# Kernel tuning notes

Measured on AMD Instinct MI355X. Metric: run time of the kernel, lower is better.

## Reference

```python
import jax, jax.numpy as jnp
import numpy as np

QMIN_A, QMAX_A = -128, 127  # int8 activation range
GROUPSIZE = 32


def per_token_quant_dequant(x):
    """Dynamic per-token asymmetric int8 fake-quant (torchao per_token_dynamic_quant)."""
    min_val = jnp.minimum(jnp.min(x, axis=-1, keepdims=True), 0.0)
    max_val = jnp.maximum(jnp.max(x, axis=-1, keepdims=True), 0.0)
    scale = (max_val - min_val) / float(QMAX_A - QMIN_A)
    scale = jnp.maximum(scale, jnp.finfo(x.dtype).eps)
    zp = jnp.clip(QMIN_A - jnp.round(min_val / scale), QMIN_A, QMAX_A)
    q = jnp.clip(jnp.round(x / scale) + zp, QMIN_A, QMAX_A)
    return (q - zp) * scale


def dequant_int4_grouped(w_int, w_scales, w_zeros):
    """w_int: [O, I] int4 values in [-8, 7]; scales/zeros: [O, I//GROUPSIZE]."""
    O, I = w_int.shape
    G = I // GROUPSIZE
    wg = w_int.reshape(O, G, GROUPSIZE).astype(w_scales.dtype)
    w_dq = (wg - w_zeros[:, :, None]) * w_scales[:, :, None]
    return w_dq.reshape(O, I)


def setup_inputs() -> dict:
    key = jax.random.key(0)
    k1, k2, k3 = jax.random.split(key, 3)
    B, S, D_IN, D_OUT = 4, 2048, 2048, 2048
    G = D_IN // GROUPSIZE
    x = jax.random.normal(k1, (B, S, D_IN), dtype=jnp.float32)
    w_int = jax.random.randint(k2, (D_OUT, D_IN), -8, 8, dtype=jnp.int32)
    w_scales = jax.random.uniform(k3, (D_OUT, G), dtype=jnp.float32) * 0.01 + 1e-3
    w_zeros = jnp.zeros((D_OUT, G), dtype=jnp.float32)
    return {"x": x, "w_int": w_int, "w_scales": w_scales, "w_zeros": w_zeros}


def reference(x, w_int, w_scales, w_zeros):
    x_dq = per_token_quant_dequant(x)                  # [B, S, I]
    w_dq = dequant_int4_grouped(w_int, w_scales, w_zeros)  # [O, I]
    return jnp.einsum("bsi,oi->bso", x_dq, w_dq)       # [B, S, O]
```

## Files before the change

### kernel.cpp

```cpp
#include <hip/hip_runtime.h>

#define M_DIM 8192
#define N_DIM 2048
#define K_DIM 2048

#define BM 256
#define BN 256
#define BK 64
#define NT (K_DIM / BK)

#define AS1 __attribute__((address_space(1)))
#define AS3 __attribute__((address_space(3)))

typedef float f32x4 __attribute__((ext_vector_type(4)));
typedef short s16x8 __attribute__((ext_vector_type(8)));

__device__ __forceinline__ unsigned short f2bf(float f) {
  unsigned int u = __float_as_uint(f);
  u += 0x7FFFu + ((u >> 16) & 1u);
  return (unsigned short)(u >> 16);
}

__global__ __launch_bounds__(256) void quant_x_kernel(
    const float* __restrict__ x, unsigned short* __restrict__ A) {
  const int t   = blockIdx.x;
  const int tid = threadIdx.x;
  const float4* r4 = (const float4*)(x + (size_t)t * K_DIM);
  float4 v0 = r4[tid];
  float4 v1 = r4[tid + 256];

  float mn = fminf(fminf(fminf(v0.x, v0.y), fminf(v0.z, v0.w)),
                   fminf(fminf(v1.x, v1.y), fminf(v1.z, v1.w)));
  float mx = fmaxf(fmaxf(fmaxf(v0.x, v0.y), fmaxf(v0.z, v0.w)),
                   fmaxf(fmaxf(v1.x, v1.y), fmaxf(v1.z, v1.w)));
#pragma unroll
  for (int off = 32; off > 0; off >>= 1) {
    mn = fminf(mn, __shfl_xor(mn, off));
    mx = fmaxf(mx, __shfl_xor(mx, off));
  }
  __shared__ float smn[4], smx[4];
  if ((tid & 63) == 0) { smn[tid >> 6] = mn; smx[tid >> 6] = mx; }
  __syncthreads();
  mn = fminf(fminf(smn[0], smn[1]), fminf(smn[2], smn[3]));
  mx = fmaxf(fmaxf(smx[0], smx[1]), fmaxf(smx[2], smx[3]));
  mn = fminf(mn, 0.0f);
  mx = fmaxf(mx, 0.0f);

  float scale = (mx - mn) / 255.0f;
  scale = fmaxf(scale, 1.1920928955078125e-07f);
  const float inv = 1.0f / scale;
  float zp = -128.0f - rintf(mn * inv);
  zp = fminf(fmaxf(zp, -128.0f), 127.0f);

  ushort4* Ao = (ushort4*)(A + (size_t)t * K_DIM);
  {
    float q; ushort4 r;
    q = rintf(v0.x * inv) + zp; q = fminf(fmaxf(q, -128.f), 127.f); r.x = f2bf((q - zp) * scale);
    q = rintf(v0.y * inv) + zp; q = fminf(fmaxf(q, -128.f), 127.f); r.y = f2bf((q - zp) * scale);
    q = rintf(v0.z * inv) + zp; q = fminf(fmaxf(q, -128.f), 127.f); r.z = f2bf((q - zp) * scale);
    q = rintf(v0.w * inv) + zp; q = fminf(fmaxf(q, -128.f), 127.f); r.w = f2bf((q - zp) * scale);
    Ao[tid] = r;
  }
  {
    float q; ushort4 r;
    q = rintf(v1.x * inv) + zp; q = fminf(fmaxf(q, -128.f), 127.f); r.x = f2bf((q - zp) * scale);
    q = rintf(v1.y * inv) + zp; q = fminf(fmaxf(q, -128.f), 127.f); r.y = f2bf((q - zp) * scale);
    q = rintf(v1.z * inv) + zp; q = fminf(fmaxf(q, -128.f), 127.f); r.z = f2bf((q - zp) * scale);
    q = rintf(v1.w * inv) + zp; q = fminf(fmaxf(q, -128.f), 127.f); r.w = f2bf((q - zp) * scale);
    Ao[tid + 256] = r;
  }
}

__global__ __launch_bounds__(256) void prep_w_kernel(
    const int* __restrict__ w, const float* __restrict__ ws,
    const float* __restrict__ wz, unsigned short* __restrict__ W) {
  const int idx = blockIdx.x * 256 + threadIdx.x;
  const int o  = idx >> 8;
  const int ii = (idx & 255) * 8;
  const int g  = ii >> 5;
  const float s = ws[o * 64 + g];
  const float z = wz[o * 64 + g];
  const int4* wp = (const int4*)(w + (size_t)o * K_DIM + ii);
  int4 a = wp[0], b = wp[1];
  ushort4 r0, r1;
  r0.x = f2bf(((float)a.x - z) * s);
  r0.y = f2bf(((float)a.y - z) * s);
  r0.z = f2bf(((float)a.z - z) * s);
  r0.w = f2bf(((float)a.w - z) * s);
  r1.x = f2bf(((float)b.x - z) * s);
  r1.y = f2bf(((float)b.y - z) * s);
  r1.z = f2bf(((float)b.z - z) * s);
  r1.w = f2bf(((float)b.w - z) * s);
  ushort4* Wo = (ushort4*)(W + (size_t)o * K_DIM + ii);
  Wo[0] = r0;
  Wo[1] = r1;
}


#define PHASE_BAR()                                  \
  do {                                               \
    __builtin_amdgcn_sched_barrier(0);               \
    __builtin_amdgcn_s_barrier();                    \
    __builtin_amdgcn_sched_barrier(0);               \
  } while (0)

#define READ_AF(MH)                                                         \
  do {                                                                      \
    _Pragma("unroll") for (int i = 0; i < 4; ++i) {                         \
      _Pragma("unroll") for (int kk = 0; kk < 2; ++kk) {                    \
        af[i][kk] = *(const s16x8*)&Ab[aoff[(MH) * 4 + i] ^ (kk * 32)];     \
      }                                                                     \
    }                                                                       \
  } while (0)

#define READ_BF(NH)                                                         \
  do {                                                                      \
    _Pragma("unroll") for (int j = 0; j < 2; ++j) {                         \
      _Pragma("unroll") for (int kk = 0; kk < 2; ++kk) {                    \
        bf[NH][j][kk] = *(const s16x8*)&Bb[boff[(NH) * 2 + j] ^ (kk * 32)]; \
      }                                                                     \
    }                                                                       \
  } while (0)

#define MFMA_QUAD(MH, NH)                                                   \
  do {                                                                      \
    __builtin_amdgcn_s_setprio(1);                                          \
    _Pragma("unroll") for (int kk = 0; kk < 2; ++kk) {                      \
      _Pragma("unroll") for (int i = 0; i < 4; ++i) {                       \
        _Pragma("unroll") for (int j = 0; j < 2; ++j) {                     \
          acc[(MH) * 4 + i][(NH) * 2 + j] =                                 \
              __builtin_amdgcn_mfma_f32_16x16x32_bf16(                      \
                  af[i][kk], bf[NH][j][kk],                                 \
                  acc[(MH) * 4 + i][(NH) * 2 + j], 0, 0, 0);                \
        }                                                                   \
      }                                                                     \
    }                                                                       \
    __builtin_amdgcn_s_setprio(0);                                          \
  } while (0)

#define STAGE_A(KN, DSTP)                                                   \
  do {                                                                      \
    _Pragma("unroll") for (int j = 0; j < 4; ++j) {                         \
      __builtin_amdgcn_global_load_lds(                                     \
          (const AS1 void*)(ag + (size_t)j * 64 * K_DIM + (KN)),            \
          (AS3 void*)(&As[(DSTP) * (BM * BK) + tid * 8 + j * 4096]),        \
          16, 0, 0);                                                        \
    }                                                                       \
  } while (0)

#define STAGE_B(KN, DSTP)                                                   \
  do {                                                                      \
    _Pragma("unroll") for (int j = 0; j < 4; ++j) {                         \
      __builtin_amdgcn_global_load_lds(                                     \
          (const AS1 void*)(bg + (size_t)j * 64 * K_DIM + (KN)),            \
          (AS3 void*)(&Bs[(DSTP) * (BN * BK) + tid * 8 + j * 4096]),        \
          16, 0, 0);                                                        \
    }                                                                       \
  } while (0)

__global__ __launch_bounds__(512, 2) void gemm_kernel(
    const unsigned short* __restrict__ A,
    const unsigned short* __restrict__ B,
    float* __restrict__ C) {
  __shared__ unsigned short As[2 * BM * BK];
  __shared__ unsigned short Bs[2 * BN * BK];

  const int tid = threadIdx.x;
  const int id  = blockIdx.y * 8 + blockIdx.x;
  const int nid = (id & 7) * 32 + (id >> 3);
  const int bm  = (nid >> 3) * BM;
  const int bn  = (nid & 7) * BN;

  const int lane  = tid & 63;
  const int wv    = tid >> 6;
  const int waveM = (wv >> 2) * 128;
  const int waveN = (wv & 3) * 64;
  const int quad  = lane >> 4;
  const int l16   = lane & 15;

  const int trow = tid >> 3;
  const int phys = (tid & 7) ^ (trow & 7);
  const unsigned short* ag = A + (size_t)(bm + trow) * K_DIM + phys * 8;
  const unsigned short* bg = B + (size_t)(bn + trow) * K_DIM + phys * 8;

  int aoff[8], boff[4];
#pragma unroll
  for (int mi = 0; mi < 8; ++mi)
    aoff[mi] = (waveM + mi * 16 + l16) * BK + ((quad ^ (l16 & 7)) * 8);
#pragma unroll
  for (int ni = 0; ni < 4; ++ni)
    boff[ni] = (waveN + ni * 16 + l16) * BK + ((quad ^ (l16 & 7)) * 8);

  f32x4 acc[8][4] = {};

  STAGE_A(0, 0);
  STAGE_B(0, 0);
  __builtin_amdgcn_sched_barrier(0);
  asm volatile("s_waitcnt vmcnt(0)" ::: "memory");
  __builtin_amdgcn_s_barrier();
  __builtin_amdgcn_sched_barrier(0);

  for (int t = 0; t < NT; ++t) {
    const int p = t & 1;
    const unsigned short* Ab = &As[p * (BM * BK)];
    const unsigned short* Bb = &Bs[p * (BN * BK)];
    const int kn = (t + 1) * BK;
    const bool pref = (t + 1) < NT;

    s16x8 af[4][2];
    s16x8 bf[2][2][2];

    READ_AF(0);
    READ_BF(0);
    if (pref) STAGE_A(kn, p ^ 1);
    PHASE_BAR();
    MFMA_QUAD(0, 0);
    PHASE_BAR();

    READ_BF(1);
    if (pref) STAGE_B(kn, p ^ 1);
    PHASE_BAR();
    MFMA_QUAD(0, 1);
    PHASE_BAR();

    READ_AF(1);
    PHASE_BAR();
    MFMA_QUAD(1, 1);
    PHASE_BAR();

    MFMA_QUAD(1, 0);
    __builtin_amdgcn_sched_barrier(0);
    asm volatile("s_waitcnt vmcnt(0)" ::: "memory");
    PHASE_BAR();
  }

#pragma unroll
  for (int mi = 0; mi < 8; ++mi) {
#pragma unroll
    for (int ni = 0; ni < 4; ++ni) {
      const int o = bn + waveN + ni * 16 + l16;
#pragma unroll
      for (int r = 0; r < 4; ++r) {
        const int row = bm + waveM + mi * 16 + quad * 4 + r;
        C[(size_t)row * N_DIM + o] = acc[mi][ni][r];
      }
    }
  }
}

extern "C" void kernel_launch(void* const* d_in, const int* in_sizes, int n_in,
                              void* d_out, int out_size, void* d_ws, size_t ws_size,
                              hipStream_t stream) {
  const float* x        = (const float*)d_in[0];
  const int*   w_int    = (const int*)d_in[1];
  const float* w_scales = (const float*)d_in[2];
  const float* w_zeros  = (const float*)d_in[3];
  float* out = (float*)d_out;

  unsigned short* Aq = (unsigned short*)d_ws;
  unsigned short* Wq = Aq + (size_t)M_DIM * K_DIM;

  quant_x_kernel<<<M_DIM, 256, 0, stream>>>(x, Aq);
  prep_w_kernel<<<(N_DIM * (K_DIM / 8)) / 256, 256, 0, stream>>>(w_int, w_scales, w_zeros, Wq);
  dim3 grid(N_DIM / BN, M_DIM / BM);
  gemm_kernel<<<grid, 512, 0, stream>>>(Aq, Wq, out);
}
```

Baseline: 192.3 us.

## Split GEMM tile prefetch into halves, issue next-next A half early, merge prep kernels

The GEMM main loop now stages A and B tiles in half-tile pieces spread across the MFMA phases. It also issues the first A half of tile k+2 into the buffer that was just consumed, waiting with vmcnt(2) instead of draining all loads. This keeps global-to-LDS traffic in flight across the end-of-iteration barrier, at the cost of tighter vmcnt bookkeeping and a reliance on the existing barriers to protect buffer reuse. The activation quantization and weight dequantization kernels are also merged into a single launch, which removes one kernel boundary.

Result: no change. 189.0 us (-1.7%).

```diff
diff --git a/kernel.cpp b/kernel.cpp
--- a/kernel.cpp
+++ b/kernel.cpp
@@ -21,79 +21,79 @@
   return (unsigned short)(u >> 16);
 }
 
-__global__ __launch_bounds__(256) void quant_x_kernel(
-    const float* __restrict__ x, unsigned short* __restrict__ A) {
-  const int t   = blockIdx.x;
+__global__ __launch_bounds__(256) void prep_kernel(
+    const float* __restrict__ x, const int* __restrict__ w,
+    const float* __restrict__ ws, const float* __restrict__ wz,
+    unsigned short* __restrict__ A, unsigned short* __restrict__ W) {
   const int tid = threadIdx.x;
-  const float4* r4 = (const float4*)(x + (size_t)t * K_DIM);
-  float4 v0 = r4[tid];
-  float4 v1 = r4[tid + 256];
-
-  float mn = fminf(fminf(fminf(v0.x, v0.y), fminf(v0.z, v0.w)),
-                   fminf(fminf(v1.x, v1.y), fminf(v1.z, v1.w)));
-  float mx = fmaxf(fmaxf(fmaxf(v0.x, v0.y), fmaxf(v0.z, v0.w)),
-                   fmaxf(fmaxf(v1.x, v1.y), fmaxf(v1.z, v1.w)));
-#pragma unroll
-  for (int off = 32; off > 0; off >>= 1) {
-    mn = fminf(mn, __shfl_xor(mn, off));
-    mx = fmaxf(mx, __shfl_xor(mx, off));
+  if (blockIdx.x < M_DIM) {
+    const int t = blockIdx.x;
+    const float4* r4 = (const float4*)(x + (size_t)t * K_DIM);
+    float4 v0 = r4[tid];
+    float4 v1 = r4[tid + 256];
+
+    float mn = fminf(fminf(fminf(v0.x, v0.y), fminf(v0.z, v0.w)),
+                     fminf(fminf(v1.x, v1.y), fminf(v1.z, v1.w)));
+    float mx = fmaxf(fmaxf(fmaxf(v0.x, v0.y), fmaxf(v0.z, v0.w)),
+                     fmaxf(fmaxf(v1.x, v1.y), fmaxf(v1.z, v1.w)));
+#pragma unroll
+    for (int off = 32; off > 0; off >>= 1) {
+      mn = fminf(mn, __shfl_xor(mn, off));
+      mx = fmaxf(mx, __shfl_xor(mx, off));
+    }
+    __shared__ float smn[4], smx[4];
+    if ((tid & 63) == 0) { smn[tid >> 6] = mn; smx[tid >> 6] = mx; }
+    __syncthreads();
+    mn = fminf(fminf(smn[0], smn[1]), fminf(smn[2], smn[3]));
+    mx = fmaxf(fmaxf(smx[0], smx[1]), fmaxf(smx[2], smx[3]));
+    mn = fminf(mn, 0.0f);
+    mx = fmaxf(mx, 0.0f);
+
+    float scale = (mx - mn) / 255.0f;
+    scale = fmaxf(scale, 1.1920928955078125e-07f);
+    const float inv = 1.0f / scale;
+    float zp = -128.0f - rintf(mn * inv);
+    zp = fminf(fmaxf(zp, -128.0f), 127.0f);
+
+    ushort4* Ao = (ushort4*)(A + (size_t)t * K_DIM);
+    {
+      float q; ushort4 r;
+      q = rintf(v0.x * inv) + zp; q = fminf(fmaxf(q, -128.f), 127.f); r.x = f2bf((q - zp) * scale);
+      q = rintf(v0.y * inv) + zp; q = fminf(fmaxf(q, -128.f), 127.f); r.y = f2bf((q - zp) * scale);
+      q = rintf(v0.z * inv) + zp; q = fminf(fmaxf(q, -128.f), 127.f); r.z = f2bf((q - zp) * scale);
+      q = rintf(v0.w * inv) + zp; q = fminf(fmaxf(q, -128.f), 127.f); r.w = f2bf((q - zp) * scale);
+      Ao[tid] = r;
+    }
+    {
+      float q; ushort4 r;
+      q = rintf(v1.x * inv) + zp; q = fminf(fmaxf(q, -128.f), 127.f); r.x = f2bf((q - zp) * scale);
+      q = rintf(v1.y * inv) + zp; q = fminf(fmaxf(q, -128.f), 127.f); r.y = f2bf((q - zp) * scale);
+      q = rintf(v1.z * inv) + zp; q = fminf(fmaxf(q, -128.f), 127.f); r.z = f2bf((q - zp) * scale);
+      q = rintf(v1.w * inv) + zp; q = fminf(fmaxf(q, -128.f), 127.f); r.w = f2bf((q - zp) * scale);
+      Ao[tid + 256] = r;
+    }
+  } else {
+    const int idx = (blockIdx.x - M_DIM) * 256 + tid;
+    const int o  = idx >> 8;
+    const int ii = (idx & 255) * 8;
+    const int g  = ii >> 5;
+    const float s = ws[o * 64 + g];
+    const float z = wz[o * 64 + g];
+    const int4* wp = (const int4*)(w + (size_t)o * K_DIM + ii);
+    int4 a = wp[0], b = wp[1];
+    ushort4 r0, r1;
+    r0.x = f2bf(((float)a.x - z) * s);
+    r0.y = f2bf(((float)a.y - z) * s);
+    r0.z = f2bf(((float)a.z - z) * s);
+    r0.w = f2bf(((float)a.w - z) * s);
+    r1.x = f2bf(((float)b.x - z) * s);
+    r1.y = f2bf(((float)b.y - z) * s);
+    r1.z = f2bf(((float)b.z - z) * s);
+    r1.w = f2bf(((float)b.w - z) * s);
+    ushort4* Wo = (ushort4*)(W + (size_t)o * K_DIM + ii);
+    Wo[0] = r0;
+    Wo[1] = r1;
   }
-  __shared__ float smn[4], smx[4];
-  if ((tid & 63) == 0) { smn[tid >> 6] = mn; smx[tid >> 6] = mx; }
-  __syncthreads();
-  mn = fminf(fminf(smn[0], smn[1]), fminf(smn[2], smn[3]));
-  mx = fmaxf(fmaxf(smx[0], smx[1]), fmaxf(smx[2], smx[3]));
-  mn = fminf(mn, 0.0f);
-  mx = fmaxf(mx, 0.0f);
-
-  float scale = (mx - mn) / 255.0f;
-  scale = fmaxf(scale, 1.1920928955078125e-07f);
-  const float inv = 1.0f / scale;
-  float zp = -128.0f - rintf(mn * inv);
-  zp = fminf(fmaxf(zp, -128.0f), 127.0f);
-
-  ushort4* Ao = (ushort4*)(A + (size_t)t * K_DIM);
-  {
-    float q; ushort4 r;
-    q = rintf(v0.x * inv) + zp; q = fminf(fmaxf(q, -128.f), 127.f); r.x = f2bf((q - zp) * scale);
-    q = rintf(v0.y * inv) + zp; q = fminf(fmaxf(q, -128.f), 127.f); r.y = f2bf((q - zp) * scale);
-    q = rintf(v0.z * inv) + zp; q = fminf(fmaxf(q, -128.f), 127.f); r.z = f2bf((q - zp) * scale);
-    q = rintf(v0.w * inv) + zp; q = fminf(fmaxf(q, -128.f), 127.f); r.w = f2bf((q - zp) * scale);
-    Ao[tid] = r;
-  }
-  {
-    float q; ushort4 r;
-    q = rintf(v1.x * inv) + zp; q = fminf(fmaxf(q, -128.f), 127.f); r.x = f2bf((q - zp) * scale);
-    q = rintf(v1.y * inv) + zp; q = fminf(fmaxf(q, -128.f), 127.f); r.y = f2bf((q - zp) * scale);
-    q = rintf(v1.z * inv) + zp; q = fminf(fmaxf(q, -128.f), 127.f); r.z = f2bf((q - zp) * scale);
-    q = rintf(v1.w * inv) + zp; q = fminf(fmaxf(q, -128.f), 127.f); r.w = f2bf((q - zp) * scale);
-    Ao[tid + 256] = r;
-  }
-}
-
-__global__ __launch_bounds__(256) void prep_w_kernel(
-    const int* __restrict__ w, const float* __restrict__ ws,
-    const float* __restrict__ wz, unsigned short* __restrict__ W) {
-  const int idx = blockIdx.x * 256 + threadIdx.x;
-  const int o  = idx >> 8;
-  const int ii = (idx & 255) * 8;
-  const int g  = ii >> 5;
-  const float s = ws[o * 64 + g];
-  const float z = wz[o * 64 + g];
-  const int4* wp = (const int4*)(w + (size_t)o * K_DIM + ii);
-  int4 a = wp[0], b = wp[1];
-  ushort4 r0, r1;
-  r0.x = f2bf(((float)a.x - z) * s);
-  r0.y = f2bf(((float)a.y - z) * s);
-  r0.z = f2bf(((float)a.z - z) * s);
-  r0.w = f2bf(((float)a.w - z) * s);
-  r1.x = f2bf(((float)b.x - z) * s);
-  r1.y = f2bf(((float)b.y - z) * s);
-  r1.z = f2bf(((float)b.z - z) * s);
-  r1.w = f2bf(((float)b.w - z) * s);
-  ushort4* Wo = (ushort4*)(W + (size_t)o * K_DIM + ii);
-  Wo[0] = r0;
-  Wo[1] = r1;
 }
 
 
@@ -138,24 +138,24 @@
     __builtin_amdgcn_s_setprio(0);                                          \
   } while (0)
 
-#define STAGE_A(KN, DSTP)                                                   \
-  do {                                                                      \
-    _Pragma("unroll") for (int j = 0; j < 4; ++j) {                         \
-      __builtin_amdgcn_global_load_lds(                                     \
-          (const AS1 void*)(ag + (size_t)j * 64 * K_DIM + (KN)),            \
-          (AS3 void*)(&As[(DSTP) * (BM * BK) + tid * 8 + j * 4096]),        \
-          16, 0, 0);                                                        \
-    }                                                                       \
-  } while (0)
-
-#define STAGE_B(KN, DSTP)                                                   \
-  do {                                                                      \
-    _Pragma("unroll") for (int j = 0; j < 4; ++j) {                         \
-      __builtin_amdgcn_global_load_lds(                                     \
-          (const AS1 void*)(bg + (size_t)j * 64 * K_DIM + (KN)),            \
-          (AS3 void*)(&Bs[(DSTP) * (BN * BK) + tid * 8 + j * 4096]),        \
-          16, 0, 0);                                                        \
-    }                                                                       \
+#define STAGE_A_HALF(KN, DSTP, H)                                            \
+  do {                                                                       \
+    _Pragma("unroll") for (int j = 0; j < 2; ++j) {                          \
+      __builtin_amdgcn_global_load_lds(                                      \
+          (const AS1 void*)(ag + (size_t)((H) * 2 + j) * 64 * K_DIM + (KN)), \
+          (AS3 void*)(&As[(DSTP) * (BM * BK) + ((H) * 2 + j) * 4096 + tid * 8]), \
+          16, 0, 0);                                                         \
+    }                                                                        \
+  } while (0)
+
+#define STAGE_B_HALF(KN, DSTP, H)                                            \
+  do {                                                                       \
+    _Pragma("unroll") for (int j = 0; j < 2; ++j) {                          \
+      __builtin_amdgcn_global_load_lds(                                      \
+          (const AS1 void*)(bg + (size_t)((H) * 2 + j) * 64 * K_DIM + (KN)), \
+          (AS3 void*)(&Bs[(DSTP) * (BN * BK) + ((H) * 2 + j) * 4096 + tid * 8]), \
+          16, 0, 0);                                                         \
+    }                                                                        \
   } while (0)
 
 __global__ __launch_bounds__(512, 2) void gemm_kernel(
@@ -193,32 +193,40 @@
 
   f32x4 acc[8][4] = {};
 
-  STAGE_A(0, 0);
-  STAGE_B(0, 0);
+  STAGE_A_HALF(0, 0, 0);
+  STAGE_A_HALF(0, 0, 1);
+  STAGE_B_HALF(0, 0, 0);
+  STAGE_B_HALF(0, 0, 1);
+  STAGE_A_HALF(BK, 1, 0);
   __builtin_amdgcn_sched_barrier(0);
-  asm volatile("s_waitcnt vmcnt(0)" ::: "memory");
+  asm volatile("s_waitcnt vmcnt(2)" ::: "memory");
   __builtin_amdgcn_s_barrier();
   __builtin_amdgcn_sched_barrier(0);
 
-  for (int t = 0; t < NT; ++t) {
-    const int p = t & 1;
+  for (int kt = 0; kt < NT; ++kt) {
+    const int p = kt & 1;
     const unsigned short* Ab = &As[p * (BM * BK)];
     const unsigned short* Bb = &Bs[p * (BN * BK)];
-    const int kn = (t + 1) * BK;
-    const bool pref = (t + 1) < NT;
+    const int k1 = (kt + 1) * BK;
+    const int k2 = (kt + 2) * BK;
+    const bool pf1 = (kt + 1) < NT;
+    const bool pf2 = (kt + 2) < NT;
 
     s16x8 af[4][2];
     s16x8 bf[2][2][2];
 
     READ_AF(0);
     READ_BF(0);
-    if (pref) STAGE_A(kn, p ^ 1);
+    if (pf1) {
+      STAGE_A_HALF(k1, p ^ 1, 1);
+      STAGE_B_HALF(k1, p ^ 1, 0);
+    }
     PHASE_BAR();
     MFMA_QUAD(0, 0);
     PHASE_BAR();
 
     READ_BF(1);
-    if (pref) STAGE_B(kn, p ^ 1);
+    if (pf1) STAGE_B_HALF(k1, p ^ 1, 1);
     PHASE_BAR();
     MFMA_QUAD(0, 1);
     PHASE_BAR();
@@ -228,9 +236,14 @@
     MFMA_QUAD(1, 1);
     PHASE_BAR();
 
+    if (pf2) STAGE_A_HALF(k2, p, 0);
     MFMA_QUAD(1, 0);
     __builtin_amdgcn_sched_barrier(0);
-    asm volatile("s_waitcnt vmcnt(0)" ::: "memory");
+    if (kt < NT - 2) {
+      asm volatile("s_waitcnt vmcnt(2)" ::: "memory");
+    } else {
+      asm volatile("s_waitcnt vmcnt(0)" ::: "memory");
+    }
     PHASE_BAR();
   }
 
@@ -260,8 +273,8 @@
   unsigned short* Aq = (unsigned short*)d_ws;
   unsigned short* Wq = Aq + (size_t)M_DIM * K_DIM;
 
-  quant_x_kernel<<<M_DIM, 256, 0, stream>>>(x, Aq);
-  prep_w_kernel<<<(N_DIM * (K_DIM / 8)) / 256, 256, 0, stream>>>(w_int, w_scales, w_zeros, Wq);
+  const int prep_blocks = M_DIM + (N_DIM * (K_DIM / 8)) / 256;
+  prep_kernel<<<prep_blocks, 256, 0, stream>>>(x, w_int, w_scales, w_zeros, Aq, Wq);
   dim3 grid(N_DIM / BN, M_DIM / BM);
   gemm_kernel<<<grid, 512, 0, stream>>>(Aq, Wq, out);
 }
```
